# Kernel optimization log

Hardware: AMD Instinct MI355X
Metric: run time of the kernel (lower is better)

The kernel has to match this reference:

```python
import jax, jax.numpy as jnp
import numpy as np

K = 1024      # num_embeddings
D = 256       # embedding_dim
BETA = 0.25
DECAY = 0.99
EPS = 1e-05


def setup_inputs() -> dict:
    key = jax.random.key(0)
    k1, k2 = jax.random.split(key)
    z_e = jax.random.normal(k1, (32, D, 32, 32), dtype=jnp.float32)
    embedding = jax.random.normal(k2, (K, D), dtype=jnp.float32)
    ema_cluster_size = jnp.zeros((K,), dtype=jnp.float32)
    ema_w = embedding  # buffer initialized as a clone of the codebook
    return {"z_e": z_e, "embedding": embedding,
            "ema_cluster_size": ema_cluster_size, "ema_w": ema_w}


def reference(z_e, embedding, ema_cluster_size, ema_w):
    B, Dd, H, W = z_e.shape
    # (B, D, H, W) -> (N, D)
    flat_z = jnp.transpose(z_e, (0, 2, 3, 1)).reshape(-1, Dd)

    # L2 distance argmin (||z||^2 + ||e||^2 - 2 z.e)
    dist = (jnp.sum(flat_z * flat_z, axis=1, keepdims=True)
            + jnp.sum(embedding * embedding, axis=1)
            - 2.0 * flat_z @ embedding.T)
    indices = jnp.argmin(dist, axis=1)  # (N,)

    # EMA update (operates on detached values; buffers updated in-place in torch)
    flat_z_sg = jax.lax.stop_gradient(flat_z)
    cluster_size = jax.ops.segment_sum(
        jnp.ones_like(indices, dtype=z_e.dtype), indices, num_segments=K)
    new_ema_cluster_size = DECAY * ema_cluster_size + (1.0 - DECAY) * cluster_size
    dw = jax.ops.segment_sum(flat_z_sg, indices, num_segments=K)  # one_hot.T @ flat_z
    new_ema_w = DECAY * ema_w + (1.0 - DECAY) * dw
    new_embedding = new_ema_w / (new_ema_cluster_size + EPS)[:, None]

    # Gather uses the *updated* codebook (torch copies into the buffer first)
    z_q_flat = new_embedding[indices]                      # (N, D)
    z_q = jnp.transpose(z_q_flat.reshape(B, H, W, Dd), (0, 3, 1, 2))

    # Straight-through estimator + commitment loss
    z_q_st = z_e + jax.lax.stop_gradient(z_q - z_e)
    vq_loss = BETA * jnp.mean((z_e - jax.lax.stop_gradient(z_q)) ** 2)

    return (z_q_st, vq_loss, indices.reshape(B, H, W),
            new_embedding, new_ema_cluster_size, new_ema_w)
```

## Files before the change

### kernel.cpp

```cpp
#include <hip/hip_runtime.h>
#include <stdint.h>

#define N_ROWS 32768
#define K_CODES 1024
#define D_DIM 256
#define NELEM 8388608

#define WS_COUNTS 0
#define WS_LOSS 1030
#define WS_ENORM 263168
#define WS_ROWBEST_BYTES 1056768
#define WS_IDX_BYTES 1318912

#define O_ZQ 0
#define O_LOSS 8388608
#define O_IDX 8388609
#define O_EMB 8421377
#define O_CS 8683521
#define O_EMAW 8684545

#define EP_BYTE_OFF 33685520

typedef _Float16 half8 __attribute__((ext_vector_type(8)));
typedef float f32x16 __attribute__((ext_vector_type(16)));

__device__ __forceinline__ unsigned int fenc(float f) {
    unsigned int u = __float_as_uint(f);
    return (u & 0x80000000u) ? ~u : (u | 0x80000000u);
}
__device__ __forceinline__ unsigned long long umin64(unsigned long long a, unsigned long long b) {
    return a < b ? a : b;
}
__device__ __forceinline__ void gll16(const void* g, void* l) {
    __builtin_amdgcn_global_load_lds((const __attribute__((address_space(1))) void*)g,
                                     (__attribute__((address_space(3))) void*)l, 16, 0, 0);
}

__global__ __launch_bounds__(256) void k_init(float* ws) {
    int i = blockIdx.x * 256 + threadIdx.x;
    if (i < 2048) ws[i] = 0.0f;
    unsigned long long* rb = (unsigned long long*)((char*)ws + WS_ROWBEST_BYTES);
    if (i < N_ROWS) rb[i] = 0xFFFFFFFFFFFFFFFFull;
}

__global__ __launch_bounds__(256) void k_conv_e(const float* __restrict__ emb,
                                                _Float16* __restrict__ Ep,
                                                float* __restrict__ enorm) {
    int k = blockIdx.x, d = threadIdx.x;
    float v = emb[k * 256 + d];
    _Float16 h = (_Float16)v;
    _Float16 l = (_Float16)(v - (float)h);
    int s = d >> 3, sub = d & 7;
    Ep[((size_t)s * 1024 + k) * 8 + sub] = h;
    Ep[((size_t)(32 + s) * 1024 + k) * 8 + sub] = l;
    float sq = v * v;
    #pragma unroll
    for (int off = 32; off >= 1; off >>= 1) sq += __shfl_down(sq, off, 64);
    __shared__ float red[4];
    if ((d & 63) == 0) red[d >> 6] = sq;
    __syncthreads();
    if (d == 0) enorm[k] = (red[0] + red[1]) + (red[2] + red[3]);
}

__global__ __launch_bounds__(256) void k_conv_z(const float* __restrict__ z_e,
                                                _Float16* __restrict__ Zp,
                                                float* __restrict__ lossacc) {
    __shared__ float lt[64 * 68];
    __shared__ float red[4];
    int t = threadIdx.x;
    int hw0 = blockIdx.x * 64, d0 = blockIdx.y * 64, b = blockIdx.z;
    const float* src = z_e + (size_t)b * 262144 + (size_t)d0 * 1024 + hw0;
    int dl = t >> 4, hl = (t & 15) * 4;
    float sq = 0.0f;
    #pragma unroll
    for (int i = 0; i < 4; i++) {
        int d = dl + i * 16;
        float4 v = *(const float4*)(src + (size_t)d * 1024 + hl);
        sq += v.x * v.x + v.y * v.y + v.z * v.z + v.w * v.w;
        lt[(hl + 0) * 68 + d] = v.x;
        lt[(hl + 1) * 68 + d] = v.y;
        lt[(hl + 2) * 68 + d] = v.z;
        lt[(hl + 3) * 68 + d] = v.w;
    }
    __syncthreads();
    int hr = t >> 2, seg = t & 3;
    int n = b * 1024 + hw0 + hr;
    int sg0 = (d0 >> 3) + seg * 2;
    half8 hi[2], lo[2];
    #pragma unroll
    for (int p = 0; p < 2; p++) {
        #pragma unroll
        for (int j = 0; j < 8; j++) {
            float v = lt[hr * 68 + seg * 16 + p * 8 + j];
            _Float16 h = (_Float16)v;
            hi[p][j] = h;
            lo[p][j] = (_Float16)(v - (float)h);
        }
    }
    *(half8*)(Zp + ((size_t)(sg0 + 0) * 32768 + n) * 8) = hi[0];
    *(half8*)(Zp + ((size_t)(sg0 + 1) * 32768 + n) * 8) = hi[1];
    *(half8*)(Zp + ((size_t)(32 + sg0) * 32768 + n) * 8) = lo[0];
    *(half8*)(Zp + ((size_t)(33 + sg0) * 32768 + n) * 8) = lo[1];
    #pragma unroll
    for (int off = 32; off >= 1; off >>= 1) sq += __shfl_down(sq, off, 64);
    if ((t & 63) == 0) red[t >> 6] = sq;
    __syncthreads();
    if (t == 0) atomicAdd(lossacc, (red[0] + red[1]) + (red[2] + red[3]));
}

__global__ __launch_bounds__(512) void k_mm(const _Float16* __restrict__ Zp,
                                            const _Float16* __restrict__ Ep,
                                            const float* __restrict__ enorm,
                                            unsigned long long* __restrict__ row_best) {
    __shared__ __align__(16) char smem[131072];

    int t = threadIdx.x;
    int lane = t & 63, wv = t >> 6;
    int b = blockIdx.x;
    int wgid = (b & 7) * 64 + (b >> 3);
    int rt = wgid >> 2;
    int ct = wgid & 3;
    int row0 = rt * 256, code0 = ct * 256;

    int wr = wv >> 2, wc = wv & 3;
    int m31 = lane & 31, ko = lane >> 5;

    f32x16 acc[4][2];
    #pragma unroll
    for (int m = 0; m < 4; m++)
        #pragma unroll
        for (int n = 0; n < 2; n++)
            #pragma unroll
            for (int r = 0; r < 16; r++) acc[m][n][r] = 0.0f;

    const char* zbase = (const char*)Zp + ((size_t)wv * 32768 + row0 + lane) * 16;
    const char* ebase = (const char*)Ep + ((size_t)wv * 1024 + code0 + lane) * 16;
    _Float16* zlds = (_Float16*)smem + wv * 256 * 8;
    _Float16* elds = (_Float16*)(smem + 32768) + wv * 256 * 8;

    auto STAGE = [&](int c, int buf) {
        int kz = (c < 8) ? c : (c - 8);
        int ge = (c < 4) ? c * 8 : (c < 8) ? (c - 4) * 8 : 32 + (c - 8) * 8;
        const char* zg = zbase + (size_t)kz * 8 * 32768 * 16;
        const char* eg = ebase + (size_t)ge * 1024 * 16;
        _Float16* zl = zlds + buf * 32768;
        _Float16* el = elds + buf * 32768;
        #pragma unroll
        for (int i = 0; i < 4; i++) {
            gll16(zg + (size_t)i * 64 * 16, zl + i * 512);
            gll16(eg + (size_t)i * 64 * 16, el + i * 512);
        }
    };

    STAGE(0, 0);
    STAGE(1, 1);
    asm volatile("s_waitcnt vmcnt(8)" ::: "memory");
    __builtin_amdgcn_s_barrier();
    asm volatile("" ::: "memory");

    for (int c = 0; c < 12; c++) {
        const _Float16* Za = (const _Float16*)(smem + (c & 1) * 65536);
        const _Float16* Ea = (const _Float16*)(smem + (c & 1) * 65536 + 32768);
        __builtin_amdgcn_s_setprio(1);
        #pragma unroll
        for (int ks = 0; ks < 4; ks++) {
            int sseg = 2 * ks + ko;
            half8 a0 = *(const half8*)(Za + (sseg * 256 + wr * 128 +  0 + m31) * 8);
            half8 a1 = *(const half8*)(Za + (sseg * 256 + wr * 128 + 32 + m31) * 8);
            half8 a2 = *(const half8*)(Za + (sseg * 256 + wr * 128 + 64 + m31) * 8);
            half8 a3 = *(const half8*)(Za + (sseg * 256 + wr * 128 + 96 + m31) * 8);
            half8 b0 = *(const half8*)(Ea + (sseg * 256 + wc * 64 +  0 + m31) * 8);
            half8 b1 = *(const half8*)(Ea + (sseg * 256 + wc * 64 + 32 + m31) * 8);
            acc[0][0] = __builtin_amdgcn_mfma_f32_32x32x16_f16(a0, b0, acc[0][0], 0, 0, 0);
            acc[0][1] = __builtin_amdgcn_mfma_f32_32x32x16_f16(a0, b1, acc[0][1], 0, 0, 0);
            acc[1][0] = __builtin_amdgcn_mfma_f32_32x32x16_f16(a1, b0, acc[1][0], 0, 0, 0);
            acc[1][1] = __builtin_amdgcn_mfma_f32_32x32x16_f16(a1, b1, acc[1][1], 0, 0, 0);
            acc[2][0] = __builtin_amdgcn_mfma_f32_32x32x16_f16(a2, b0, acc[2][0], 0, 0, 0);
            acc[2][1] = __builtin_amdgcn_mfma_f32_32x32x16_f16(a2, b1, acc[2][1], 0, 0, 0);
            acc[3][0] = __builtin_amdgcn_mfma_f32_32x32x16_f16(a3, b0, acc[3][0], 0, 0, 0);
            acc[3][1] = __builtin_amdgcn_mfma_f32_32x32x16_f16(a3, b1, acc[3][1], 0, 0, 0);
        }
        __builtin_amdgcn_s_setprio(0);
        asm volatile("s_waitcnt lgkmcnt(0)" ::: "memory");
        __builtin_amdgcn_s_barrier();
        if (c < 10) STAGE(c + 2, c & 1);
        if (c < 11) {
            if (c < 10) asm volatile("s_waitcnt vmcnt(8)" ::: "memory");
            else        asm volatile("s_waitcnt vmcnt(0)" ::: "memory");
            __builtin_amdgcn_s_barrier();
            asm volatile("" ::: "memory");
        }
    }

    unsigned long long* slot = (unsigned long long*)smem;
    float en0 = enorm[code0 + wc * 64 + m31];
    float en1 = enorm[code0 + wc * 64 + 32 + m31];
    unsigned int col0 = code0 + wc * 64 + m31;
    unsigned int col1 = col0 + 32;

    if (wc == 0) {
        #pragma unroll
        for (int m = 0; m < 4; m++)
            #pragma unroll
            for (int j = 0; j < 16; j++) {
                int row = wr * 128 + m * 32 + 4 * ko + (j & 3) + 8 * (j >> 2);
                unsigned long long p0 = ((unsigned long long)fenc(en0 - 2.0f * acc[m][0][j]) << 32) | col0;
                unsigned long long p1 = ((unsigned long long)fenc(en1 - 2.0f * acc[m][1][j]) << 32) | col1;
                slot[row * 32 + ((m31 + row) & 31)] = umin64(p0, p1);
            }
    }
    __syncthreads();
    if (wc != 0) {
        #pragma unroll
        for (int m = 0; m < 4; m++)
            #pragma unroll
            for (int j = 0; j < 16; j++) {
                int row = wr * 128 + m * 32 + 4 * ko + (j & 3) + 8 * (j >> 2);
                unsigned long long p0 = ((unsigned long long)fenc(en0 - 2.0f * acc[m][0][j]) << 32) | col0;
                unsigned long long p1 = ((unsigned long long)fenc(en1 - 2.0f * acc[m][1][j]) << 32) | col1;
                atomicMin(&slot[row * 32 + ((m31 + row) & 31)], umin64(p0, p1));
            }
    }
    __syncthreads();
    if (t < 256) {
        unsigned long long mm = slot[t * 32 + (t & 31)];
        #pragma unroll
        for (int i = 1; i < 32; i++) mm = umin64(mm, slot[t * 32 + ((i + t) & 31)]);
        atomicMin(&row_best[row0 + t], mm);
    }
}

__global__ __launch_bounds__(256) void k_fin_idx(const unsigned long long* __restrict__ rb,
                                                 int* __restrict__ idxs,
                                                 float* __restrict__ counts,
                                                 float* __restrict__ out) {
    __shared__ float hist[K_CODES];
    int t = threadIdx.x;
    #pragma unroll
    for (int j = 0; j < 4; j++) hist[j * 256 + t] = 0.0f;
    __syncthreads();
    int i = blockIdx.x * 256 + t;
    int id = (int)(rb[i] & 0xFFFFFFFFull);
    idxs[i] = id;
    out[O_IDX + i] = (float)id;
    atomicAdd(&hist[id], 1.0f);
    __syncthreads();
    #pragma unroll
    for (int j = 0; j < 4; j++) {
        float h = hist[j * 256 + t];
        if (h != 0.0f) atomicAdd(&counts[j * 256 + t], h);
    }
}

__global__ __launch_bounds__(256) void k_dw(const float* __restrict__ z_e,
                                            const int* __restrict__ idxs,
                                            float* __restrict__ part) {
    __shared__ float acc[K_CODES];
    int t = threadIdx.x;
    int s = blockIdx.x;
    int d = blockIdx.y;
    #pragma unroll
    for (int j = 0; j < 4; j++) acc[j * 256 + t] = 0.0f;
    __syncthreads();
    #pragma unroll
    for (int i = 0; i < 4; i++) {
        int b = s * 4 + i;
        int4 id4 = *(const int4*)(idxs + b * 1024 + t * 4);
        float4 v = *(const float4*)(z_e + (size_t)b * 262144 + (size_t)d * 1024 + t * 4);
        atomicAdd(&acc[id4.x], v.x);
        atomicAdd(&acc[id4.y], v.y);
        atomicAdd(&acc[id4.z], v.z);
        atomicAdd(&acc[id4.w], v.w);
    }
    __syncthreads();
    float* pr = part + ((size_t)s * 256 + d) * 1024;
    #pragma unroll
    for (int j = 0; j < 4; j++) pr[j * 256 + t] = acc[j * 256 + t];
}

__global__ __launch_bounds__(256) void k_red(const float* __restrict__ part,
                                             const float* __restrict__ ema_cs,
                                             const float* __restrict__ ema_w,
                                             const float* __restrict__ counts,
                                             float* __restrict__ lossacc,
                                             float* __restrict__ out) {
    __shared__ float tile[64 * 69];
    __shared__ float csl[64];
    __shared__ float craw[64];
    __shared__ float red[4];
    int t = threadIdx.x;
    int k0 = blockIdx.x * 64, d0 = blockIdx.y * 64;
    int dr = t >> 4, kc = t & 15;
    float4 sum[4] = {};
    for (int s = 0; s < 8; s++) {
        const float* pb = part + ((size_t)s * 256 + d0) * 1024 + k0 + kc * 4;
        #pragma unroll
        for (int q = 0; q < 4; q++) {
            float4 v = *(const float4*)(pb + (size_t)(dr + 16 * q) * 1024);
            sum[q].x += v.x; sum[q].y += v.y; sum[q].z += v.z; sum[q].w += v.w;
        }
    }
    if (t < 64) {
        float c = counts[k0 + t];
        craw[t] = c;
        csl[t] = 0.99f * ema_cs[k0 + t] + 0.01f * c;
    }
    #pragma unroll
    for (int q = 0; q < 4; q++) {
        float* p = tile + (dr + 16 * q) * 69 + kc * 4;
        p[0] = sum[q].x; p[1] = sum[q].y; p[2] = sum[q].z; p[3] = sum[q].w;
    }
    __syncthreads();
    int kk = t >> 2, dq = t & 3;
    int k = k0 + kk;
    float inv = 1.0f / (csl[kk] + 1e-5f);
    float cr = craw[kk];
    float lterm = 0.0f;
    #pragma unroll
    for (int j4 = 0; j4 < 4; j4++) {
        int dd = dq * 16 + j4 * 4;
        size_t kd = (size_t)k * 256 + d0 + dd;
        float4 w = *(const float4*)(ema_w + kd);
        float s0 = tile[(dd + 0) * 69 + kk];
        float s1 = tile[(dd + 1) * 69 + kk];
        float s2 = tile[(dd + 2) * 69 + kk];
        float s3 = tile[(dd + 3) * 69 + kk];
        float4 nw;
        nw.x = 0.99f * w.x + 0.01f * s0;
        nw.y = 0.99f * w.y + 0.01f * s1;
        nw.z = 0.99f * w.z + 0.01f * s2;
        nw.w = 0.99f * w.w + 0.01f * s3;
        *(float4*)(out + O_EMAW + kd) = nw;
        float4 ne = {nw.x * inv, nw.y * inv, nw.z * inv, nw.w * inv};
        *(float4*)(out + O_EMB + kd) = ne;
        lterm += ne.x * (cr * ne.x - 2.0f * s0);
        lterm += ne.y * (cr * ne.y - 2.0f * s1);
        lterm += ne.z * (cr * ne.z - 2.0f * s2);
        lterm += ne.w * (cr * ne.w - 2.0f * s3);
    }
    if (blockIdx.y == 0 && t < 64) out[O_CS + k0 + t] = csl[t];
    #pragma unroll
    for (int off = 32; off >= 1; off >>= 1) lterm += __shfl_down(lterm, off, 64);
    if ((t & 63) == 0) red[t >> 6] = lterm;
    __syncthreads();
    if (t == 0) atomicAdd(lossacc, (red[0] + red[1]) + (red[2] + red[3]));
}

__global__ __launch_bounds__(256) void k_bcast(const int* __restrict__ idxs,
                                               const float* __restrict__ lossacc,
                                               float* __restrict__ out) {
    __shared__ float lt[64 * 68];
    __shared__ int sid[64];
    int t = threadIdx.x;
    int hw0 = blockIdx.x * 64, d0 = blockIdx.y * 64, b = blockIdx.z;
    if (t < 64) sid[t] = idxs[b * 1024 + hw0 + t];
    __syncthreads();
    int r = t >> 2, c = t & 3;
    const float* nrow = out + O_EMB + (size_t)sid[r] * 256 + d0;
    #pragma unroll
    for (int it = 0; it < 4; it++) {
        int dd = it * 16 + c * 4;
        float4 q = *(const float4*)(nrow + dd);
        float* p = lt + r * 68 + dd;
        p[0] = q.x; p[1] = q.y; p[2] = q.z; p[3] = q.w;
    }
    __syncthreads();
    int dl = t >> 4, hl = (t & 15) * 4;
    float* dst = out + O_ZQ + (size_t)b * 262144 + (size_t)d0 * 1024 + hw0;
    #pragma unroll
    for (int i = 0; i < 4; i++) {
        int d = dl + i * 16;
        float4 w;
        w.x = lt[(hl + 0) * 68 + d];
        w.y = lt[(hl + 1) * 68 + d];
        w.z = lt[(hl + 2) * 68 + d];
        w.w = lt[(hl + 3) * 68 + d];
        *(float4*)(dst + (size_t)d * 1024 + hl) = w;
    }
    if (blockIdx.x == 0 && blockIdx.y == 0 && blockIdx.z == 0 && t == 0)
        out[O_LOSS] = lossacc[0] * 2.9802322387695312e-08f;
}

extern "C" void kernel_launch(void* const* d_in, const int* in_sizes, int n_in,
                              void* d_out, int out_size, void* d_ws, size_t ws_size,
                              hipStream_t stream) {
    const float* z_e = (const float*)d_in[0];
    const float* emb = (const float*)d_in[1];
    const float* ema_cs = (const float*)d_in[2];
    const float* ema_w = (const float*)d_in[3];
    float* out = (float*)d_out;
    float* ws = (float*)d_ws;

    float* counts = ws + WS_COUNTS;
    float* lossacc = ws + WS_LOSS;
    float* enorm = ws + WS_ENORM;
    unsigned long long* row_best = (unsigned long long*)((char*)d_ws + WS_ROWBEST_BYTES);
    int* idxs = (int*)((char*)d_ws + WS_IDX_BYTES);

    _Float16* Zp = (_Float16*)d_out;
    _Float16* Ep = (_Float16*)((char*)d_out + EP_BYTE_OFF);
    float* part = (float*)d_out;

    k_init<<<128, 256, 0, stream>>>(ws);
    k_conv_e<<<1024, 256, 0, stream>>>(emb, Ep, enorm);
    k_conv_z<<<dim3(16, 4, 32), 256, 0, stream>>>(z_e, Zp, lossacc);
    k_mm<<<512, 512, 0, stream>>>(Zp, Ep, enorm, row_best);
    k_fin_idx<<<128, 256, 0, stream>>>(row_best, idxs, counts, out);
    k_dw<<<dim3(8, 256), 256, 0, stream>>>(z_e, idxs, part);
    k_red<<<dim3(16, 4), 256, 0, stream>>>(part, ema_cs, ema_w, counts, lossacc, out);
    k_bcast<<<dim3(16, 4, 32), 256, 0, stream>>>(idxs, lossacc, out);
}
```

Before: 244.2 us.

## Interleave per-quarter global-to-LDS staging with MFMA steps in distance matmul

Replaces the whole-tile double-buffer staging with quarter-tile loads spread across the four k-substeps of each tile. Each substep now issues a global-to-LDS load, then runs its MFMAs, so memory traffic overlaps compute more finely. The wait is now a vmcnt(12) after every substep. In exchange there are more barriers per tile, and the modulo-12 wraparound issues redundant loads at the end of the loop that must be drained before the epilogue.

```diff
diff --git a/kernel.cpp b/kernel.cpp
--- a/kernel.cpp
+++ b/kernel.cpp
@@ -125,6 +125,12 @@
     int wr = wv >> 2, wc = wv & 3;
     int m31 = lane & 31, ko = lane >> 5;
 
+    int sh = wv >> 2;
+    int r0 = (wv & 3) * 64;
+
+    const char* zgw = (const char*)Zp + ((size_t)row0 + r0 + lane) * 16;
+    const char* egw = (const char*)Ep + ((size_t)code0 + r0 + lane) * 16;
+
     f32x16 acc[4][2];
     #pragma unroll
     for (int m = 0; m < 4; m++)
@@ -133,44 +139,44 @@
             #pragma unroll
             for (int r = 0; r < 16; r++) acc[m][n][r] = 0.0f;
 
-    const char* zbase = (const char*)Zp + ((size_t)wv * 32768 + row0 + lane) * 16;
-    const char* ebase = (const char*)Ep + ((size_t)wv * 1024 + code0 + lane) * 16;
-    _Float16* zlds = (_Float16*)smem + wv * 256 * 8;
-    _Float16* elds = (_Float16*)(smem + 32768) + wv * 256 * 8;
-
-    auto STAGE = [&](int c, int buf) {
-        int kz = (c < 8) ? c : (c - 8);
-        int ge = (c < 4) ? c * 8 : (c < 8) ? (c - 4) * 8 : 32 + (c - 8) * 8;
-        const char* zg = zbase + (size_t)kz * 8 * 32768 * 16;
-        const char* eg = ebase + (size_t)ge * 1024 * 16;
-        _Float16* zl = zlds + buf * 32768;
-        _Float16* el = elds + buf * 32768;
-        #pragma unroll
-        for (int i = 0; i < 4; i++) {
-            gll16(zg + (size_t)i * 64 * 16, zl + i * 512);
-            gll16(eg + (size_t)i * 64 * 16, el + i * 512);
-        }
+    auto zsegbase = [](int tt) { return (tt < 8 ? tt : tt - 8) * 8; };
+    auto gesegbase = [](int tt) { return tt < 4 ? tt * 8 : (tt < 8 ? (tt - 4) * 8 : 32 + (tt - 8) * 8); };
+
+    auto STAGEQ = [&](int st, int sq) {
+        int s = 2 * sq + sh;
+        const char* zg = zgw + ((size_t)(zsegbase(st) + s) * 32768) * 16;
+        const char* eg = egw + ((size_t)(gesegbase(st) + s) * 1024) * 16;
+        char* zl = smem + (st & 1) * 65536 + (s * 256 + r0) * 16;
+        char* el = smem + (st & 1) * 65536 + 32768 + (s * 256 + r0) * 16;
+        gll16(zg, zl);
+        gll16(eg, el);
     };
 
-    STAGE(0, 0);
-    STAGE(1, 1);
-    asm volatile("s_waitcnt vmcnt(8)" ::: "memory");
+    STAGEQ(0, 0); STAGEQ(0, 1); STAGEQ(0, 2); STAGEQ(0, 3);
+    STAGEQ(1, 0); STAGEQ(1, 1); STAGEQ(1, 2);
+    asm volatile("s_waitcnt vmcnt(12)" ::: "memory");
     __builtin_amdgcn_s_barrier();
     asm volatile("" ::: "memory");
 
-    for (int c = 0; c < 12; c++) {
-        const _Float16* Za = (const _Float16*)(smem + (c & 1) * 65536);
-        const _Float16* Ea = (const _Float16*)(smem + (c & 1) * 65536 + 32768);
-        __builtin_amdgcn_s_setprio(1);
-        #pragma unroll
-        for (int ks = 0; ks < 4; ks++) {
-            int sseg = 2 * ks + ko;
+    for (int tt = 0; tt < 12; tt++) {
+        const _Float16* Za = (const _Float16*)(smem + (tt & 1) * 65536);
+        const _Float16* Ea = (const _Float16*)(smem + (tt & 1) * 65536 + 32768);
+        int t1 = tt + 1; if (t1 >= 12) t1 -= 12;
+        int t2 = tt + 2; if (t2 >= 12) t2 -= 12;
+        #pragma unroll
+        for (int q = 0; q < 4; q++) {
+            if (q == 0) STAGEQ(t1, 3);
+            else        STAGEQ(t2, q - 1);
+            int sseg = 2 * q + ko;
             half8 a0 = *(const half8*)(Za + (sseg * 256 + wr * 128 +  0 + m31) * 8);
             half8 a1 = *(const half8*)(Za + (sseg * 256 + wr * 128 + 32 + m31) * 8);
             half8 a2 = *(const half8*)(Za + (sseg * 256 + wr * 128 + 64 + m31) * 8);
             half8 a3 = *(const half8*)(Za + (sseg * 256 + wr * 128 + 96 + m31) * 8);
             half8 b0 = *(const half8*)(Ea + (sseg * 256 + wc * 64 +  0 + m31) * 8);
             half8 b1 = *(const half8*)(Ea + (sseg * 256 + wc * 64 + 32 + m31) * 8);
+            __builtin_amdgcn_s_barrier();
+            asm volatile("s_waitcnt lgkmcnt(0)" ::: "memory");
+            __builtin_amdgcn_s_setprio(1);
             acc[0][0] = __builtin_amdgcn_mfma_f32_32x32x16_f16(a0, b0, acc[0][0], 0, 0, 0);
             acc[0][1] = __builtin_amdgcn_mfma_f32_32x32x16_f16(a0, b1, acc[0][1], 0, 0, 0);
             acc[1][0] = __builtin_amdgcn_mfma_f32_32x32x16_f16(a1, b0, acc[1][0], 0, 0, 0);
@@ -179,18 +185,15 @@
             acc[2][1] = __builtin_amdgcn_mfma_f32_32x32x16_f16(a2, b1, acc[2][1], 0, 0, 0);
             acc[3][0] = __builtin_amdgcn_mfma_f32_32x32x16_f16(a3, b0, acc[3][0], 0, 0, 0);
             acc[3][1] = __builtin_amdgcn_mfma_f32_32x32x16_f16(a3, b1, acc[3][1], 0, 0, 0);
-        }
-        __builtin_amdgcn_s_setprio(0);
-        asm volatile("s_waitcnt lgkmcnt(0)" ::: "memory");
-        __builtin_amdgcn_s_barrier();
-        if (c < 10) STAGE(c + 2, c & 1);
-        if (c < 11) {
-            if (c < 10) asm volatile("s_waitcnt vmcnt(8)" ::: "memory");
-            else        asm volatile("s_waitcnt vmcnt(0)" ::: "memory");
+            __builtin_amdgcn_s_setprio(0);
+            asm volatile("s_waitcnt vmcnt(12)" ::: "memory");
             __builtin_amdgcn_s_barrier();
             asm volatile("" ::: "memory");
         }
     }
+    asm volatile("s_waitcnt vmcnt(0)" ::: "memory");
+    __builtin_amdgcn_s_barrier();
+    asm volatile("" ::: "memory");
 
     unsigned long long* slot = (unsigned long long*)smem;
     float en0 = enorm[code0 + wc * 64 + m31];
```

Result: no change. 241.5 us (-1.1%).

## Fold init into codebook conversion and compute dw without split partials

Applied to the files above, without the earlier changes.

Workspace zeroing and row_best initialisation move into k_conv_e, which removes one kernel launch. k_dw now uses one 512-thread block per embedding dimension that loops over all 32 batches and writes the final dw directly, so the 8-way partial buffer and the summation pass in k_red go away. In exchange k_dw runs only 256 blocks, each with a longer serial loop and more LDS atomic contention per block, which lowers parallelism on a large GPU.

```diff
diff --git a/kernel.cpp b/kernel.cpp
--- a/kernel.cpp
+++ b/kernel.cpp
@@ -36,17 +36,16 @@
                                      (__attribute__((address_space(3))) void*)l, 16, 0, 0);
 }
 
-__global__ __launch_bounds__(256) void k_init(float* ws) {
-    int i = blockIdx.x * 256 + threadIdx.x;
-    if (i < 2048) ws[i] = 0.0f;
-    unsigned long long* rb = (unsigned long long*)((char*)ws + WS_ROWBEST_BYTES);
-    if (i < N_ROWS) rb[i] = 0xFFFFFFFFFFFFFFFFull;
-}
-
 __global__ __launch_bounds__(256) void k_conv_e(const float* __restrict__ emb,
                                                 _Float16* __restrict__ Ep,
-                                                float* __restrict__ enorm) {
+                                                float* __restrict__ enorm,
+                                                float* __restrict__ ws) {
     int k = blockIdx.x, d = threadIdx.x;
+    int gid = k * 256 + d;
+    if (gid < 2048) ws[gid] = 0.0f;
+    unsigned long long* rb = (unsigned long long*)((char*)ws + WS_ROWBEST_BYTES);
+    if (gid < N_ROWS) rb[gid] = 0xFFFFFFFFFFFFFFFFull;
+
     float v = emb[k * 256 + d];
     _Float16 h = (_Float16)v;
     _Float16 l = (_Float16)(v - (float)h);
@@ -252,33 +251,28 @@
     }
 }
 
-__global__ __launch_bounds__(256) void k_dw(const float* __restrict__ z_e,
+__global__ __launch_bounds__(512) void k_dw(const float* __restrict__ z_e,
                                             const int* __restrict__ idxs,
-                                            float* __restrict__ part) {
+                                            float* __restrict__ dw) {
     __shared__ float acc[K_CODES];
     int t = threadIdx.x;
-    int s = blockIdx.x;
-    int d = blockIdx.y;
-    #pragma unroll
-    for (int j = 0; j < 4; j++) acc[j * 256 + t] = 0.0f;
-    __syncthreads();
-    #pragma unroll
-    for (int i = 0; i < 4; i++) {
-        int b = s * 4 + i;
-        int4 id4 = *(const int4*)(idxs + b * 1024 + t * 4);
-        float4 v = *(const float4*)(z_e + (size_t)b * 262144 + (size_t)d * 1024 + t * 4);
-        atomicAdd(&acc[id4.x], v.x);
-        atomicAdd(&acc[id4.y], v.y);
-        atomicAdd(&acc[id4.z], v.z);
-        atomicAdd(&acc[id4.w], v.w);
-    }
-    __syncthreads();
-    float* pr = part + ((size_t)s * 256 + d) * 1024;
-    #pragma unroll
-    for (int j = 0; j < 4; j++) pr[j * 256 + t] = acc[j * 256 + t];
-}
-
-__global__ __launch_bounds__(256) void k_red(const float* __restrict__ part,
+    int d = blockIdx.x;
+    #pragma unroll
+    for (int j = 0; j < 2; j++) acc[j * 512 + t] = 0.0f;
+    __syncthreads();
+    for (int b = 0; b < 32; b++) {
+        int2 id2 = *(const int2*)(idxs + b * 1024 + t * 2);
+        float2 v = *(const float2*)(z_e + (size_t)b * 262144 + (size_t)d * 1024 + t * 2);
+        atomicAdd(&acc[id2.x], v.x);
+        atomicAdd(&acc[id2.y], v.y);
+    }
+    __syncthreads();
+    float* pr = dw + (size_t)d * 1024;
+    #pragma unroll
+    for (int j = 0; j < 2; j++) pr[j * 512 + t] = acc[j * 512 + t];
+}
+
+__global__ __launch_bounds__(256) void k_red(const float* __restrict__ dw,
                                              const float* __restrict__ ema_cs,
                                              const float* __restrict__ ema_w,
                                              const float* __restrict__ counts,
@@ -291,15 +285,6 @@
     int t = threadIdx.x;
     int k0 = blockIdx.x * 64, d0 = blockIdx.y * 64;
     int dr = t >> 4, kc = t & 15;
-    float4 sum[4] = {};
-    for (int s = 0; s < 8; s++) {
-        const float* pb = part + ((size_t)s * 256 + d0) * 1024 + k0 + kc * 4;
-        #pragma unroll
-        for (int q = 0; q < 4; q++) {
-            float4 v = *(const float4*)(pb + (size_t)(dr + 16 * q) * 1024);
-            sum[q].x += v.x; sum[q].y += v.y; sum[q].z += v.z; sum[q].w += v.w;
-        }
-    }
     if (t < 64) {
         float c = counts[k0 + t];
         craw[t] = c;
@@ -307,8 +292,9 @@
     }
     #pragma unroll
     for (int q = 0; q < 4; q++) {
+        float4 v = *(const float4*)(dw + (size_t)(d0 + dr + 16 * q) * 1024 + k0 + kc * 4);
         float* p = tile + (dr + 16 * q) * 69 + kc * 4;
-        p[0] = sum[q].x; p[1] = sum[q].y; p[2] = sum[q].z; p[3] = sum[q].w;
+        p[0] = v.x; p[1] = v.y; p[2] = v.z; p[3] = v.w;
     }
     __syncthreads();
     int kk = t >> 2, dq = t & 3;
@@ -399,14 +385,13 @@
 
     _Float16* Zp = (_Float16*)d_out;
     _Float16* Ep = (_Float16*)((char*)d_out + EP_BYTE_OFF);
-    float* part = (float*)d_out;
-
-    k_init<<<128, 256, 0, stream>>>(ws);
-    k_conv_e<<<1024, 256, 0, stream>>>(emb, Ep, enorm);
+    float* dw = (float*)d_out;
+
+    k_conv_e<<<1024, 256, 0, stream>>>(emb, Ep, enorm, ws);
     k_conv_z<<<dim3(16, 4, 32), 256, 0, stream>>>(z_e, Zp, lossacc);
     k_mm<<<512, 512, 0, stream>>>(Zp, Ep, enorm, row_best);
     k_fin_idx<<<128, 256, 0, stream>>>(row_best, idxs, counts, out);
-    k_dw<<<dim3(8, 256), 256, 0, stream>>>(z_e, idxs, part);
-    k_red<<<dim3(16, 4), 256, 0, stream>>>(part, ema_cs, ema_w, counts, lossacc, out);
+    k_dw<<<256, 512, 0, stream>>>(z_e, idxs, dw);
+    k_red<<<dim3(16, 4), 256, 0, stream>>>(dw, ema_cs, ema_w, counts, lossacc, out);
     k_bcast<<<dim3(16, 4, 32), 256, 0, stream>>>(idxs, lossacc, out);
 }
```

New measurement: 236.0 us. -3.4%, faster.
